# Kernel optimization log

Hardware: AMD Instinct MI355X
Metric: run time of the kernel (lower is better)

## Reference

```python
import jax, jax.numpy as jnp
import numpy as np

N, L, F, C, H, D = 2, 512, 128, 64, 12, 16
INF = 1e5
SQ29 = float(np.sqrt(2.0 / 9.0))
SCALE = float(np.sqrt(1.0 / 3.0))
EPS_DIR = 1e-4
LN_EPS = 1e-5


def setup_inputs() -> dict:
    key = jax.random.key(0)
    ks = jax.random.split(key, 16)
    s = 0.02
    return {
        "R": jax.random.normal(ks[0], (N, L, 3, 3), jnp.float32),
        "t": jax.random.normal(ks[1], (N, L, 3), jnp.float32),
        "p_CB": jax.random.normal(ks[2], (N, L, 3), jnp.float32),
        "x": jax.random.normal(ks[3], (N, L, F), jnp.float32),
        "z": jax.random.normal(ks[4], (N, L, L, C), jnp.float32),
        "mask": jax.random.randint(ks[5], (N, L), 0, 2).astype(bool),
        "Wq": jax.random.normal(ks[6], (H * D, F), jnp.float32) * s,
        "Wk": jax.random.normal(ks[7], (H * D, F), jnp.float32) * s,
        "Wv": jax.random.normal(ks[8], (H * D, F), jnp.float32) * s,
        "Wpb": jax.random.normal(ks[9], (H, C), jnp.float32) * s,
        "gamma_raw": jnp.full((1, 1, 1, H), float(np.log(np.e - 1.0)), jnp.float32),
        "Wout": jax.random.normal(ks[10], (F, H * C + H * D + H * 7), jnp.float32) * s,
        "bout": jnp.zeros((F,), jnp.float32),
        "ln_w": jnp.ones((F,), jnp.float32),
        "ln_b": jnp.zeros((F,), jnp.float32),
    }


def reference(R, t, p_CB, x, z, mask, Wq, Wk, Wv, Wpb, gamma_raw, Wout, bout, ln_w, ln_b):
    # --- logits ---
    q = (x @ Wq.T).reshape(N, L, H, D)  # (N,L,H,D)
    k = (x @ Wk.T).reshape(N, L, H, D)
    v = (x @ Wv.T).reshape(N, L, H, D)
    logits_node = jnp.einsum('nihd,njhd->nijh', q, k)
    logits_pair = jnp.einsum('nijc,hc->nijh', z, Wpb)
    # CB squared distances, identical for all heads -> broadcast over H
    d2 = jnp.sum((p_CB[:, :, None, :] - p_CB[:, None, :, :]) ** 2, axis=-1)[..., None]  # (N,L,L,1)
    gamma = jax.nn.softplus(gamma_raw)  # (1,1,1,H)
    logits_beta = d2 * (-gamma * SQ29 / 2.0)
    logits = (logits_node + logits_pair + logits_beta) * SCALE
    # --- masked softmax over axis j (2) ---
    mask_row = mask[:, :, None, None]
    mask_pair = mask_row & mask[:, None, :, None]
    logits = jnp.where(mask_pair, logits, logits - INF)
    alpha = jax.nn.softmax(logits, axis=2)
    alpha = jnp.where(mask_row, alpha, jnp.zeros_like(alpha))  # (N,L,L,H)
    # --- pair aggregation ---
    feat_p2n = jnp.einsum('nijh,nijc->nihc', alpha, z).reshape(N, L, H * C)
    # --- node aggregation ---
    feat_node = jnp.einsum('nijh,njhd->nihd', alpha, v).reshape(N, L, H * D)
    # --- beta (CB point) aggregation ---
    aggr = jnp.einsum('nijh,njc->nihc', alpha, p_CB)  # (N,L,H,3) in global frame
    local = jnp.einsum('nlji,nlhj->nlhi', R, aggr - t[:, :, None, :])  # global_to_local: R^T (q - t)
    dist = jnp.linalg.norm(local, axis=-1)  # (N,L,H)
    direction = local / (dist[..., None] + EPS_DIR)
    feat_spatial = jnp.concatenate(
        [local.reshape(N, L, -1), dist.reshape(N, L, -1), direction.reshape(N, L, -1)], axis=-1)
    # --- output transform + residual layernorm ---
    feat_all = jnp.concatenate([feat_p2n, feat_node, feat_spatial], axis=-1) @ Wout.T + bout
    feat_all = jnp.where(mask[:, :, None], feat_all, 0.0)
    y = x + feat_all
    mu = jnp.mean(y, axis=-1, keepdims=True)
    var = jnp.var(y, axis=-1, keepdims=True)
    return (y - mu) / jnp.sqrt(var + LN_EPS) * ln_w + ln_b
```

## Files before the change

### kernel.cpp

```cpp
#include <hip/hip_runtime.h>
#include <hip/hip_bf16.h>

constexpr int NB   = 2;
constexpr int LL   = 512;
constexpr int FF   = 128;
constexpr int CC   = 64;
constexpr int HH   = 12;
constexpr int DD   = 16;
constexpr int HD   = HH * DD;
constexpr int FEAT = HH*CC + HH*DD + HH*7;
constexpr float INFV   = 100000.0f;
constexpr float SCALEF = 0.57735026918962576f;
constexpr float SQ29H  = 0.23570226039551584f;

__global__ __launch_bounds__(192) void qkv_kernel(
    const float* __restrict__ xg, const float* __restrict__ Wq,
    const float* __restrict__ Wk, const float* __restrict__ Wv,
    float* __restrict__ q_ws, float* __restrict__ kT4, float* __restrict__ vT)
{
    const int row = blockIdx.x;
    const int n = row >> 9, i = row & 511;
    const int t = threadIdx.x;
    __shared__ __align__(16) float sx[FF];
    __shared__ __align__(16) float sw[3*HD*20];

    if (t < FF) sx[t] = xg[(size_t)row*FF + t];

    float aq = 0.f, ak = 0.f, av = 0.f;
    for (int ft = 0; ft < 8; ++ft) {
        __syncthreads();
        #pragma unroll
        for (int m = 0; m < 3; ++m) {
            const float* W = (m == 0) ? Wq : ((m == 1) ? Wk : Wv);
            #pragma unroll
            for (int p = 0; p < 4; ++p) {
                const int r = (t >> 2) + 48*p, q = t & 3;
                float4 v = *(const float4*)(W + (size_t)r*FF + ft*16 + q*4);
                *(float4*)&sw[m*3840 + r*20 + q*4] = v;
            }
        }
        __syncthreads();
        const float* xf = &sx[ft*16];
        const float* wq = &sw[0*3840 + t*20];
        const float* wk = &sw[1*3840 + t*20];
        const float* wv = &sw[2*3840 + t*20];
        #pragma unroll
        for (int f4 = 0; f4 < 4; ++f4) {
            float4 xv = *(const float4*)&xf[f4*4];
            float4 a = *(const float4*)&wq[f4*4];
            float4 b = *(const float4*)&wk[f4*4];
            float4 c = *(const float4*)&wv[f4*4];
            aq += xv.x*a.x + xv.y*a.y + xv.z*a.z + xv.w*a.w;
            ak += xv.x*b.x + xv.y*b.y + xv.z*b.z + xv.w*b.w;
            av += xv.x*c.x + xv.y*c.y + xv.z*c.z + xv.w*c.w;
        }
    }
    q_ws[(size_t)row*HD + t] = aq;
    kT4[(((size_t)n*48 + (t >> 2))*LL + i)*4 + (t & 3)] = ak;
    vT[((size_t)n*HD + t)*LL + i] = av;
}

__global__ __launch_bounds__(512, 2) void attn_kernel(
    const float* __restrict__ Rg, const float* __restrict__ tg, const float* __restrict__ pg,
    const float* __restrict__ xg, const float* __restrict__ zg, const int* __restrict__ maskg,
    const float* __restrict__ Wpbg, const float* __restrict__ gammag,
    const float* __restrict__ Woutg, const float* __restrict__ boutg,
    const float* __restrict__ lnwg, const float* __restrict__ lnbg,
    const float* __restrict__ q_ws, const float* __restrict__ kT4, const float* __restrict__ vT,
    float* __restrict__ outg)
{
    const int row = blockIdx.x;
    const int n = row >> 9;
    const int tid = threadIdx.x;

    __shared__ __align__(16) float s_exp[HH*LL];
    __shared__ __align__(16) float s_big[4*768];
    __shared__ __align__(16) float s_q[HD];
    __shared__ __align__(16) float s_x[FF];
    __shared__ __align__(16) float s_y[FF];
    __shared__ __align__(16) float s_f[FEAT];
    __shared__ float s_aggr[36];
    __shared__ float s_inv[HH];
    __shared__ float s_coef[HH];
    __shared__ float s_geo[15];
    __shared__ float s_red[2];

    if (tid < FF) s_x[tid] = xg[(size_t)row*FF + tid];
    if (tid >= 128 && tid < 128 + HD) s_q[tid-128] = q_ws[(size_t)row*HD + (tid-128)];
    for (int o = tid; o < HH*CC; o += 512) s_big[o] = Wpbg[o];
    if (tid >= 320 && tid < 332) {
        float g = gammag[tid-320];
        float gamma = log1pf(__expf(fminf(g, 80.0f)));
        s_coef[tid-320] = -gamma * SQ29H;
    }
    if (tid >= 332 && tid < 335) s_geo[tid-332] = pg[(size_t)row*3 + (tid-332)];
    if (tid >= 335 && tid < 338) s_geo[3 + tid-335] = tg[(size_t)row*3 + (tid-335)];
    if (tid >= 338 && tid < 347) s_geo[6 + tid-338] = Rg[(size_t)row*9 + (tid-338)];
    const int mi = maskg[row];
    __syncthreads();

    if (mi) {
        {
            const int j = tid;
            float acc[HH];
            #pragma unroll
            for (int h = 0; h < HH; ++h) acc[h] = 0.f;

            const float* zr = zg + ((size_t)row*LL + j)*CC;
            #pragma unroll
            for (int c4 = 0; c4 < CC/4; ++c4) {
                float4 zv = *(const float4*)(zr + c4*4);
                #pragma unroll
                for (int h = 0; h < HH; ++h) {
                    float4 w = *(const float4*)&s_big[h*CC + c4*4];
                    acc[h] += zv.x*w.x + zv.y*w.y + zv.z*w.z + zv.w*w.w;
                }
            }
            const float* kb = kT4 + ((size_t)(n*48)*LL + j)*4;
            #pragma unroll
            for (int hd4 = 0; hd4 < HD/4; ++hd4) {
                float4 q4 = *(const float4*)&s_q[hd4*4];
                float4 k4 = *(const float4*)(kb + (size_t)hd4*LL*4);
                acc[hd4 >> 2] += q4.x*k4.x + q4.y*k4.y + q4.z*k4.z + q4.w*k4.w;
            }
            const float* pj = pg + ((size_t)n*LL + j)*3;
            float e0 = s_geo[0]-pj[0];
            float e1 = s_geo[1]-pj[1];
            float e2 = s_geo[2]-pj[2];
            float d2 = e0*e0 + e1*e1 + e2*e2;
            const float sub = maskg[n*LL + j] ? 0.0f : INFV;
            #pragma unroll
            for (int h = 0; h < HH; ++h) {
                float lg = (acc[h] + d2*s_coef[h]) * SCALEF - sub;
                s_exp[h*LL + j] = __expf(fminf(lg, 80.0f));
            }
        }
        __syncthreads();

        {
            const int wv = tid >> 6, lane = tid & 63;
            for (int h = wv; h < HH; h += 8) {
                float s = 0.f;
                #pragma unroll
                for (int r = 0; r < 8; ++r) s += s_exp[h*LL + lane + (r<<6)];
                #pragma unroll
                for (int off = 32; off > 0; off >>= 1) s += __shfl_xor(s, off, 64);
                if (lane == 0) s_inv[h] = 1.0f / fmaxf(s, 1e-30f);
            }
        }
        __syncthreads();

        {
            const int wv = tid >> 6, lane = tid & 63;
            if (wv < 4) {
                const int c = lane, q4v = wv;
                float acc[HH];
                #pragma unroll
                for (int h = 0; h < HH; ++h) acc[h] = 0.f;
                const float* zb = zg + ((size_t)row*LL + q4v*128)*CC + c;
                const float* ep = s_exp + q4v*128;
                #pragma unroll 2
                for (int jj = 0; jj < 128; ++jj) {
                    float zv = zb[(size_t)jj*CC];
                    #pragma unroll
                    for (int h = 0; h < HH; ++h) acc[h] += ep[h*LL + jj] * zv;
                }
                #pragma unroll
                for (int h = 0; h < HH; ++h) s_big[q4v*768 + h*64 + c] = acc[h];
            } else if (tid < 448) {
                const int hd = tid - 256;
                const float* vb = vT + ((size_t)n*HD + hd)*LL;
                const float* ep = s_exp + (hd >> 4)*LL;
                float a = 0.f;
                #pragma unroll 2
                for (int j4 = 0; j4 < 128; ++j4) {
                    float4 vv = *(const float4*)(vb + j4*4);
                    float4 av = *(const float4*)(ep + j4*4);
                    a += vv.x*av.x + vv.y*av.y + vv.z*av.z + vv.w*av.w;
                }
                s_f[768 + hd] = a * s_inv[hd >> 4];
            } else {
                const int o = tid - 448;
                if (o < 36) {
                    const int h = o / 3, ax = o - h*3;
                    const float* pb = pg + (size_t)n*LL*3 + ax;
                    const float* ep = s_exp + h*LL;
                    float a = 0.f;
                    #pragma unroll 4
                    for (int j = 0; j < LL; ++j) a += ep[j] * pb[(size_t)j*3];
                    s_aggr[o] = a * s_inv[h];
                }
            }
        }
        __syncthreads();

        for (int o = tid; o < 768; o += 512)
            s_f[o] = (s_big[o] + s_big[768+o] + s_big[1536+o] + s_big[2304+o]) * s_inv[o >> 6];
        if (tid >= 500) {
            const int h = tid - 500;
            float m0 = s_aggr[h*3+0] - s_geo[3];
            float m1 = s_aggr[h*3+1] - s_geo[4];
            float m2 = s_aggr[h*3+2] - s_geo[5];
            const float* Rm = &s_geo[6];
            float l0 = Rm[0]*m0 + Rm[3]*m1 + Rm[6]*m2;
            float l1 = Rm[1]*m0 + Rm[4]*m1 + Rm[7]*m2;
            float l2 = Rm[2]*m0 + Rm[5]*m1 + Rm[8]*m2;
            float dist = sqrtf(l0*l0 + l1*l1 + l2*l2);
            float idn = 1.0f/(dist + 1e-4f);
            s_f[960 + h*3+0] = l0; s_f[960 + h*3+1] = l1; s_f[960 + h*3+2] = l2;
            s_f[996 + h] = dist;
            s_f[1008 + h*3+0] = l0*idn; s_f[1008 + h*3+1] = l1*idn; s_f[1008 + h*3+2] = l2*idn;
        }
        __syncthreads();

        {
            const int f = tid & 127, q4 = tid >> 7;
            const float* wr = Woutg + (size_t)f * FEAT;
            float acc = 0.f;
            for (int kk = q4*4; kk < FEAT; kk += 16) {
                float4 fv = *(const float4*)&s_f[kk];
                float4 wvv = *(const float4*)(wr + kk);
                acc += fv.x*wvv.x + fv.y*wvv.y + fv.z*wvv.z + fv.w*wvv.w;
            }
            s_big[q4*FF + f] = acc;
        }
        __syncthreads();
        if (tid < FF)
            s_y[tid] = s_x[tid] + boutg[tid]
                     + s_big[tid] + s_big[FF + tid] + s_big[2*FF + tid] + s_big[3*FF + tid];
    } else {
        if (tid < FF) s_y[tid] = s_x[tid];
    }
    __syncthreads();

    if (tid < 64) {
        float a = s_y[tid], b = s_y[tid + 64];
        float s1 = a + b, s2 = a*a + b*b;
        #pragma unroll
        for (int off = 32; off > 0; off >>= 1) {
            s1 += __shfl_xor(s1, off, 64);
            s2 += __shfl_xor(s2, off, 64);
        }
        if (tid == 0) { s_red[0] = s1; s_red[1] = s2; }
    }
    __syncthreads();
    if (tid < FF) {
        float mu  = s_red[0] * (1.0f/FF);
        float var = s_red[1] * (1.0f/FF) - mu*mu;
        float vv = (s_y[tid] - mu) * rsqrtf(fmaxf(var, 0.0f) + 1e-5f);
        vv = vv * lnwg[tid] + lnbg[tid];
        outg[(size_t)row*FF + tid] = vv;
    }
}

extern "C" void kernel_launch(void* const* d_in, const int* in_sizes, int n_in,
                              void* d_out, int out_size, void* d_ws, size_t ws_size,
                              hipStream_t stream) {
    const float* Rg    = (const float*)d_in[0];
    const float* tg    = (const float*)d_in[1];
    const float* pg    = (const float*)d_in[2];
    const float* xg    = (const float*)d_in[3];
    const float* zg    = (const float*)d_in[4];
    const int*   maskg = (const int*)d_in[5];
    const float* Wq    = (const float*)d_in[6];
    const float* Wk    = (const float*)d_in[7];
    const float* Wv    = (const float*)d_in[8];
    const float* Wpb   = (const float*)d_in[9];
    const float* gam   = (const float*)d_in[10];
    const float* Wout  = (const float*)d_in[11];
    const float* bout  = (const float*)d_in[12];
    const float* lnw   = (const float*)d_in[13];
    const float* lnb   = (const float*)d_in[14];
    float* outp = (float*)d_out;

    float* q_ws = (float*)d_ws;
    float* kT4  = q_ws + (size_t)NB*LL*HD;
    float* vT   = kT4  + (size_t)NB*LL*HD;

    qkv_kernel<<<NB*LL, HD, 0, stream>>>(xg, Wq, Wk, Wv, q_ws, kT4, vT);
    attn_kernel<<<NB*LL, 512, 0, stream>>>(Rg, tg, pg, xg, zg, maskg,
                                           Wpb, gam, Wout, bout, lnw, lnb,
                                           q_ws, kT4, vT, outp);
}
```

Baseline: 327.2 us.

## Batch QKV rows per block, pad softmax buffer, reduce partials with LDS atomics

The QKV projection kernel now computes four rows per block, so each staged weight tile is reused four times and vT is written as float4. The attention kernel pads the exp buffer rows to avoid LDS bank conflicts and reads it as float4 in the z aggregation. It replaces the four partial buffers with shared-memory atomicAdd into one accumulator. It also reduces the output projection with lane shuffles instead of an extra sync, and raises the launch-bounds occupancy hint from 2 to 8. The higher occupancy hint can force register spills, and the LDS atomics add contention.

Result: no change. 333.0 us (+1.8%).

```diff
diff --git a/kernel.cpp b/kernel.cpp
--- a/kernel.cpp
+++ b/kernel.cpp
@@ -3,6 +3,7 @@
 
 constexpr int NB   = 2;
 constexpr int LL   = 512;
+constexpr int LLP  = 516;
 constexpr int FF   = 128;
 constexpr int CC   = 64;
 constexpr int HH   = 12;
@@ -18,15 +19,17 @@
     const float* __restrict__ Wk, const float* __restrict__ Wv,
     float* __restrict__ q_ws, float* __restrict__ kT4, float* __restrict__ vT)
 {
-    const int row = blockIdx.x;
-    const int n = row >> 9, i = row & 511;
+    const int b = blockIdx.x;
     const int t = threadIdx.x;
-    __shared__ __align__(16) float sx[FF];
+    __shared__ __align__(16) float sx[4*FF];
     __shared__ __align__(16) float sw[3*HD*20];
 
-    if (t < FF) sx[t] = xg[(size_t)row*FF + t];
-
-    float aq = 0.f, ak = 0.f, av = 0.f;
+    for (int o = t; o < 4*FF; o += 192) sx[o] = xg[(size_t)b*4*FF + o];
+
+    float aq[4] = {0.f,0.f,0.f,0.f};
+    float ak[4] = {0.f,0.f,0.f,0.f};
+    float av[4] = {0.f,0.f,0.f,0.f};
+
     for (int ft = 0; ft < 8; ++ft) {
         __syncthreads();
         #pragma unroll
@@ -40,27 +43,34 @@
             }
         }
         __syncthreads();
-        const float* xf = &sx[ft*16];
         const float* wq = &sw[0*3840 + t*20];
         const float* wk = &sw[1*3840 + t*20];
         const float* wv = &sw[2*3840 + t*20];
         #pragma unroll
         for (int f4 = 0; f4 < 4; ++f4) {
-            float4 xv = *(const float4*)&xf[f4*4];
             float4 a = *(const float4*)&wq[f4*4];
-            float4 b = *(const float4*)&wk[f4*4];
-            float4 c = *(const float4*)&wv[f4*4];
-            aq += xv.x*a.x + xv.y*a.y + xv.z*a.z + xv.w*a.w;
-            ak += xv.x*b.x + xv.y*b.y + xv.z*b.z + xv.w*b.w;
-            av += xv.x*c.x + xv.y*c.y + xv.z*c.z + xv.w*c.w;
-        }
-    }
-    q_ws[(size_t)row*HD + t] = aq;
-    kT4[(((size_t)n*48 + (t >> 2))*LL + i)*4 + (t & 3)] = ak;
-    vT[((size_t)n*HD + t)*LL + i] = av;
+            float4 bq = *(const float4*)&wk[f4*4];
+            float4 cq = *(const float4*)&wv[f4*4];
+            #pragma unroll
+            for (int r = 0; r < 4; ++r) {
+                float4 xv = *(const float4*)&sx[r*FF + ft*16 + f4*4];
+                aq[r] += xv.x*a.x  + xv.y*a.y  + xv.z*a.z  + xv.w*a.w;
+                ak[r] += xv.x*bq.x + xv.y*bq.y + xv.z*bq.z + xv.w*bq.w;
+                av[r] += xv.x*cq.x + xv.y*cq.y + xv.z*cq.z + xv.w*cq.w;
+            }
+        }
+    }
+    const int n = (b*4) >> 9, i0 = (b*4) & 511;
+    #pragma unroll
+    for (int r = 0; r < 4; ++r) {
+        const int row = b*4 + r, i = i0 + r;
+        q_ws[(size_t)row*HD + t] = aq[r];
+        kT4[(((size_t)n*48 + (t >> 2))*LL + i)*4 + (t & 3)] = ak[r];
+    }
+    *(float4*)&vT[((size_t)n*HD + t)*LL + i0] = make_float4(av[0], av[1], av[2], av[3]);
 }
 
-__global__ __launch_bounds__(512, 2) void attn_kernel(
+__global__ __launch_bounds__(512, 8) void attn_kernel(
     const float* __restrict__ Rg, const float* __restrict__ tg, const float* __restrict__ pg,
     const float* __restrict__ xg, const float* __restrict__ zg, const int* __restrict__ maskg,
     const float* __restrict__ Wpbg, const float* __restrict__ gammag,
@@ -73,8 +83,8 @@
     const int n = row >> 9;
     const int tid = threadIdx.x;
 
-    __shared__ __align__(16) float s_exp[HH*LL];
-    __shared__ __align__(16) float s_big[4*768];
+    __shared__ __align__(16) float s_exp[HH*LLP];
+    __shared__ __align__(16) float s_wacc[HH*CC];
     __shared__ __align__(16) float s_q[HD];
     __shared__ __align__(16) float s_x[FF];
     __shared__ __align__(16) float s_y[FF];
@@ -87,7 +97,7 @@
 
     if (tid < FF) s_x[tid] = xg[(size_t)row*FF + tid];
     if (tid >= 128 && tid < 128 + HD) s_q[tid-128] = q_ws[(size_t)row*HD + (tid-128)];
-    for (int o = tid; o < HH*CC; o += 512) s_big[o] = Wpbg[o];
+    for (int o = tid; o < HH*CC; o += 512) s_wacc[o] = Wpbg[o];
     if (tid >= 320 && tid < 332) {
         float g = gammag[tid-320];
         float gamma = log1pf(__expf(fminf(g, 80.0f)));
@@ -112,7 +122,7 @@
                 float4 zv = *(const float4*)(zr + c4*4);
                 #pragma unroll
                 for (int h = 0; h < HH; ++h) {
-                    float4 w = *(const float4*)&s_big[h*CC + c4*4];
+                    float4 w = *(const float4*)&s_wacc[h*CC + c4*4];
                     acc[h] += zv.x*w.x + zv.y*w.y + zv.z*w.z + zv.w*w.w;
                 }
             }
@@ -132,7 +142,7 @@
             #pragma unroll
             for (int h = 0; h < HH; ++h) {
                 float lg = (acc[h] + d2*s_coef[h]) * SCALEF - sub;
-                s_exp[h*LL + j] = __expf(fminf(lg, 80.0f));
+                s_exp[h*LLP + j] = __expf(fminf(lg, 80.0f));
             }
         }
         __syncthreads();
@@ -142,11 +152,12 @@
             for (int h = wv; h < HH; h += 8) {
                 float s = 0.f;
                 #pragma unroll
-                for (int r = 0; r < 8; ++r) s += s_exp[h*LL + lane + (r<<6)];
+                for (int r = 0; r < 8; ++r) s += s_exp[h*LLP + lane + (r<<6)];
                 #pragma unroll
                 for (int off = 32; off > 0; off >>= 1) s += __shfl_xor(s, off, 64);
                 if (lane == 0) s_inv[h] = 1.0f / fmaxf(s, 1e-30f);
             }
+            if (tid < 384) *(float2*)&s_wacc[tid*2] = make_float2(0.f, 0.f);
         }
         __syncthreads();
 
@@ -160,23 +171,29 @@
                 const float* zb = zg + ((size_t)row*LL + q4v*128)*CC + c;
                 const float* ep = s_exp + q4v*128;
                 #pragma unroll 2
-                for (int jj = 0; jj < 128; ++jj) {
-                    float zv = zb[(size_t)jj*CC];
+                for (int jj = 0; jj < 128; jj += 4) {
+                    float z0 = zb[(size_t)(jj+0)*CC];
+                    float z1 = zb[(size_t)(jj+1)*CC];
+                    float z2 = zb[(size_t)(jj+2)*CC];
+                    float z3 = zb[(size_t)(jj+3)*CC];
                     #pragma unroll
-                    for (int h = 0; h < HH; ++h) acc[h] += ep[h*LL + jj] * zv;
-                }
-                #pragma unroll
-                for (int h = 0; h < HH; ++h) s_big[q4v*768 + h*64 + c] = acc[h];
+                    for (int h = 0; h < HH; ++h) {
+                        float4 e = *(const float4*)&ep[h*LLP + jj];
+                        acc[h] += e.x*z0 + e.y*z1 + e.z*z2 + e.w*z3;
+                    }
+                }
+                #pragma unroll
+                for (int h = 0; h < HH; ++h) atomicAdd(&s_wacc[h*64 + c], acc[h]);
             } else if (tid < 448) {
                 const int hd = tid - 256;
                 const float* vb = vT + ((size_t)n*HD + hd)*LL;
-                const float* ep = s_exp + (hd >> 4)*LL;
+                const float* ep = s_exp + (hd >> 4)*LLP;
                 float a = 0.f;
-                #pragma unroll 2
+                #pragma unroll 4
                 for (int j4 = 0; j4 < 128; ++j4) {
                     float4 vv = *(const float4*)(vb + j4*4);
-                    float4 av = *(const float4*)(ep + j4*4);
-                    a += vv.x*av.x + vv.y*av.y + vv.z*av.z + vv.w*av.w;
+                    float4 ev = *(const float4*)(ep + j4*4);
+                    a += vv.x*ev.x + vv.y*ev.y + vv.z*ev.z + vv.w*ev.w;
                 }
                 s_f[768 + hd] = a * s_inv[hd >> 4];
             } else {
@@ -184,7 +201,7 @@
                 if (o < 36) {
                     const int h = o / 3, ax = o - h*3;
                     const float* pb = pg + (size_t)n*LL*3 + ax;
-                    const float* ep = s_exp + h*LL;
+                    const float* ep = s_exp + h*LLP;
                     float a = 0.f;
                     #pragma unroll 4
                     for (int j = 0; j < LL; ++j) a += ep[j] * pb[(size_t)j*3];
@@ -195,7 +212,7 @@
         __syncthreads();
 
         for (int o = tid; o < 768; o += 512)
-            s_f[o] = (s_big[o] + s_big[768+o] + s_big[1536+o] + s_big[2304+o]) * s_inv[o >> 6];
+            s_f[o] = s_wacc[o] * s_inv[o >> 6];
         if (tid >= 500) {
             const int h = tid - 500;
             float m0 = s_aggr[h*3+0] - s_geo[3];
@@ -214,20 +231,18 @@
         __syncthreads();
 
         {
-            const int f = tid & 127, q4 = tid >> 7;
+            const int f = tid >> 2, q4 = tid & 3;
             const float* wr = Woutg + (size_t)f * FEAT;
             float acc = 0.f;
             for (int kk = q4*4; kk < FEAT; kk += 16) {
-                float4 fv = *(const float4*)&s_f[kk];
+                float4 fv  = *(const float4*)&s_f[kk];
                 float4 wvv = *(const float4*)(wr + kk);
                 acc += fv.x*wvv.x + fv.y*wvv.y + fv.z*wvv.z + fv.w*wvv.w;
             }
-            s_big[q4*FF + f] = acc;
-        }
-        __syncthreads();
-        if (tid < FF)
-            s_y[tid] = s_x[tid] + boutg[tid]
-                     + s_big[tid] + s_big[FF + tid] + s_big[2*FF + tid] + s_big[3*FF + tid];
+            acc += __shfl_xor(acc, 1, 64);
+            acc += __shfl_xor(acc, 2, 64);
+            if (q4 == 0) s_y[f] = s_x[f] + boutg[f] + acc;
+        }
     } else {
         if (tid < FF) s_y[tid] = s_x[tid];
     }
@@ -277,7 +292,7 @@
     float* kT4  = q_ws + (size_t)NB*LL*HD;
     float* vT   = kT4  + (size_t)NB*LL*HD;
 
-    qkv_kernel<<<NB*LL, HD, 0, stream>>>(xg, Wq, Wk, Wv, q_ws, kT4, vT);
+    qkv_kernel<<<NB*LL/4, HD, 0, stream>>>(xg, Wq, Wk, Wv, q_ws, kT4, vT);
     attn_kernel<<<NB*LL, 512, 0, stream>>>(Rg, tg, pg, xg, zg, maskg,
                                            Wpb, gam, Wout, bout, lnw, lnb,
                                            q_ws, kT4, vT, outp);
```
